# Optimization experiments

Hardware: AMD Instinct MI355X
Metric: run time of the kernel (lower is better)

## Reference

```python
import jax, jax.numpy as jnp
import numpy as np

HIDDEN = 1024
NUM_HEADS = 16
HEAD_DIM = HIDDEN // NUM_HEADS
LOCAL_WINDOW = 64
GLOBAL_WINDOW = 256
NEG_INF = -1.0e9


def _strided_mask(seq_len: int) -> jnp.ndarray:
    # Faithful vectorization of the torch loop:
    #   mask[i, max(0,i-w//2):min(S,i+w//2)] = 1  -> band j in [i-32, i+32)
    #   mask[i, ::stride] = 1, stride = max(1, S // global_window)
    i = jnp.arange(seq_len)[:, None]
    j = jnp.arange(seq_len)[None, :]
    half = LOCAL_WINDOW // 2
    local = (j >= i - half) & (j < i + half)
    stride = max(1, seq_len // GLOBAL_WINDOW)
    strided = (j % stride) == 0
    return local | strided  # bool [S, S]


def setup_inputs() -> dict:
    key = jax.random.key(0)
    ks = jax.random.split(key, 11)
    B, S, H = 2, 2048, HIDDEN
    scale = 1.0 / np.sqrt(H)
    inp = {
        "query": jax.random.normal(ks[0], (B, S, H), dtype=jnp.float32),
        "key": jax.random.normal(ks[1], (B, S, H), dtype=jnp.float32),
        "value": jax.random.normal(ks[2], (B, S, H), dtype=jnp.float32),
        # nn.Linear weights are [out, in]; y = x @ W.T + b
        "Wq": jax.random.normal(ks[3], (H, H), dtype=jnp.float32) * scale,
        "bq": jnp.zeros((H,), dtype=jnp.float32),
        "Wk": jax.random.normal(ks[4], (H, H), dtype=jnp.float32) * scale,
        "bk": jnp.zeros((H,), dtype=jnp.float32),
        "Wv": jax.random.normal(ks[5], (H, H), dtype=jnp.float32) * scale,
        "bv": jnp.zeros((H,), dtype=jnp.float32),
        "Wo": jax.random.normal(ks[6], (H, H), dtype=jnp.float32) * scale,
        "bo": jnp.zeros((H,), dtype=jnp.float32),
    }
    return inp


def reference(query, key, value, Wq, bq, Wk, bk, Wv, bv, Wo, bo):
    B, S, H = query.shape
    nH, dH = NUM_HEADS, HEAD_DIM
    scale = 1.0 / np.sqrt(dH)

    def split_heads(x):  # [B,S,H] -> [B,nH,S,dH]
        return x.reshape(B, S, nH, dH).transpose(0, 2, 1, 3)

    Q = split_heads(query @ Wq.T + bq)
    K = split_heads(key @ Wk.T + bk)
    V = split_heads(value @ Wv.T + bv)

    scores = jnp.einsum("bhqd,bhkd->bhqk", Q, K) * scale
    mask = _strided_mask(S)[None, None, :, :]
    scores = jnp.where(mask, scores, NEG_INF)
    attn = jax.nn.softmax(scores, axis=-1)
    # dropout is identity in eval mode
    context = jnp.einsum("bhqk,bhkd->bhqd", attn, V)
    context = context.transpose(0, 2, 1, 3).reshape(B, S, H)
    output = context @ Wo.T + bo
    return output, attn
```

## Files before the change

kernel.cpp:

```cpp
#include <hip/hip_runtime.h>

typedef unsigned int uint;
typedef unsigned short ushort_t;
typedef __bf16 bf16x8 __attribute__((ext_vector_type(8)));
typedef float f32x4 __attribute__((ext_vector_type(4)));

__device__ __forceinline__ int imin(int a, int b){ return a<b?a:b; }
__device__ __forceinline__ int imax(int a, int b){ return a>b?a:b; }

__device__ __forceinline__ ushort_t f2b(float f){
  uint u = __builtin_bit_cast(uint, f);
  u += 0x7FFFu + ((u>>16)&1u);
  return (ushort_t)(u>>16);
}
__device__ __forceinline__ float b2f(ushort_t s){
  uint u = ((uint)s)<<16;
  return __builtin_bit_cast(float, u);
}
__device__ __forceinline__ f32x4 fz4(){ f32x4 z; z[0]=0.f; z[1]=0.f; z[2]=0.f; z[3]=0.f; return z; }

__device__ __forceinline__ void gload16(const void* g, void* lds){
  __builtin_amdgcn_global_load_lds(
      (const __attribute__((address_space(1))) void*)g,
      (__attribute__((address_space(3))) void*)lds,
      16, 0, 0);
}

struct CJob { const float* src; ushort_t* dst; int nvec; };

__global__ __launch_bounds__(256) void convert_k(CJob j0, CJob j1, CJob j2,
                                                 CJob j3, CJob j4, CJob j5)
{
  CJob jb;
  switch (blockIdx.y){
    case 0: jb=j0; break; case 1: jb=j1; break; case 2: jb=j2; break;
    case 3: jb=j3; break; case 4: jb=j4; break; default: jb=j5; break;
  }
  int stride = gridDim.x*256;
  for (int i = blockIdx.x*256 + threadIdx.x; i < jb.nvec; i += stride){
    const float4* s = (const float4*)(jb.src + (size_t)i*8);
    float4 v0 = s[0], v1 = s[1];
    uint4 pk;
    pk.x = (uint)f2b(v0.x) | ((uint)f2b(v0.y)<<16);
    pk.y = (uint)f2b(v0.z) | ((uint)f2b(v0.w)<<16);
    pk.z = (uint)f2b(v1.x) | ((uint)f2b(v1.y)<<16);
    pk.w = (uint)f2b(v1.z) | ((uint)f2b(v1.w)<<16);
    *(uint4*)(jb.dst + (size_t)i*8) = pk;
  }
}

struct GArg { const ushort_t* A; const ushort_t* W; const float* bias; void* O; };

template<bool OBF16>
__global__ __launch_bounds__(256) void gemm_nt(GArg g0, GArg g1, GArg g2)
{
  GArg g = (blockIdx.z==0) ? g0 : ((blockIdx.z==1) ? g1 : g2);
  __shared__ __align__(16) ushort_t As[128*32];
  __shared__ __align__(16) ushort_t Bs[128*32];
  const int tid  = threadIdx.x;
  const int lane = tid & 63;
  const int w    = tid >> 6;
  const int ml   = lane & 15, quad = lane >> 4;

  int lid = blockIdx.x + 8*blockIdx.y;
  int t   = (lid & 7)*32 + (lid >> 3);
  const int m0 = (t >> 3)*128, n0 = (t & 7)*128;
  const int wm = (w>>1)*64, wn = (w&1)*64;

  const int srow = lane >> 2;
  const int scol = ((lane & 3) ^ ((lane >> 3) & 3))*8;
  const int rA0 = w*16, rA1 = 64 + w*16;
  const ushort_t* gA = g.A + (size_t)m0*1024;
  const ushort_t* gB = g.W + (size_t)n0*1024;
  const int sxor = (quad ^ ((ml >> 1) & 3))*8;

  f32x4 acc[4][4];
  #pragma unroll
  for (int i=0;i<4;i++)
    #pragma unroll
    for (int j=0;j<4;j++) acc[i][j]=fz4();

  for (int kt=0; kt<32; ++kt){
    int kof = kt*32 + scol;
    gload16(gA + (size_t)(rA0+srow)*1024 + kof, &As[rA0*32]);
    gload16(gA + (size_t)(rA1+srow)*1024 + kof, &As[rA1*32]);
    gload16(gB + (size_t)(rA0+srow)*1024 + kof, &Bs[rA0*32]);
    gload16(gB + (size_t)(rA1+srow)*1024 + kof, &Bs[rA1*32]);
    __syncthreads();

    bf16x8 af[4], bfr[4];
    #pragma unroll
    for (int t4=0;t4<4;t4++)
      af[t4]  = __builtin_bit_cast(bf16x8, *(const uint4*)&As[(wm + t4*16 + ml)*32 + sxor]);
    #pragma unroll
    for (int t4=0;t4<4;t4++)
      bfr[t4] = __builtin_bit_cast(bf16x8, *(const uint4*)&Bs[(wn + t4*16 + ml)*32 + sxor]);
    #pragma unroll
    for (int ti=0;ti<4;ti++)
      #pragma unroll
      for (int tj=0;tj<4;tj++)
        acc[ti][tj] = __builtin_amdgcn_mfma_f32_16x16x32_bf16(af[ti], bfr[tj], acc[ti][tj], 0,0,0);
    __syncthreads();
  }
  #pragma unroll
  for (int tj=0;tj<4;tj++){
    int gcol = n0 + wn + tj*16 + ml;
    float bv = g.bias[gcol];
    #pragma unroll
    for (int ti=0;ti<4;ti++){
      int growb = m0 + wm + ti*16 + quad*4;
      #pragma unroll
      for (int r=0;r<4;r++){
        float val = acc[ti][tj][r] + bv;
        size_t off = (size_t)(growb + r)*1024 + gcol;
        if (OBF16) ((ushort_t*)g.O)[off] = f2b(val);
        else       ((float*)g.O)[off]    = val;
      }
    }
  }
}

#define SW2 360
__global__ __launch_bounds__(128) void attn_k(
    const ushort_t* Qb, const ushort_t* Kb, const ushort_t* Vb,
    ushort_t* Ctxb, float* attn_out)
{
  __shared__ ushort_t stash[32*SW2];
  __shared__ float invl[32];
  const int lane = threadIdx.x & 63;
  const int w    = threadIdx.x >> 6;
  const int ml   = lane & 15, quad = lane >> 4;
  int lid = blockIdx.x + 64*(blockIdx.y + 16*blockIdx.z);
  int tt  = (lid & 7)*256 + (lid >> 3);
  const int tile = tt & 63, h = (tt >> 6) & 15, b = tt >> 10;
  const int i0  = tile*32;
  const int jl0 = i0 - 32;
  const int rb  = 16*w;
  const size_t bh = (size_t)b*2048*1024 + (size_t)h*64;

  bf16x8 aq0, aq1;
  {
    const ushort_t* qp = Qb + bh + (size_t)(i0 + rb + ml)*1024 + quad*8;
    aq0 = __builtin_bit_cast(bf16x8, *(const uint4*)qp);
    aq1 = __builtin_bit_cast(bf16x8, *(const uint4*)(qp + 32));
  }
  float lsum[4] = {0.f,0.f,0.f,0.f};
  for (int c=0;c<22;c++){
    int j  = (c<16) ? (128*c + 8*ml) : (jl0 + 16*(c-16) + ml);
    int jc = imin(imax(j,0),2047);
    const ushort_t* kp = Kb + bh + (size_t)jc*1024 + quad*8;
    bf16x8 kb0 = __builtin_bit_cast(bf16x8, *(const uint4*)kp);
    bf16x8 kb1 = __builtin_bit_cast(bf16x8, *(const uint4*)(kp + 32));
    f32x4 sc = fz4();
    sc = __builtin_amdgcn_mfma_f32_16x16x32_bf16(aq0, kb0, sc, 0,0,0);
    sc = __builtin_amdgcn_mfma_f32_16x16x32_bf16(aq1, kb1, sc, 0,0,0);
    int slot = 16*c + ml;
    #pragma unroll
    for (int r=0;r<4;r++){
      int rl = rb + quad*4 + r;
      int i  = i0 + rl;
      bool valid = (c<16) ? true :
        ((j>=0) && (j<2048) && ((j&7)!=0) && (j >= i-32) && (j < i+32));
      float e = valid ? __expf(sc[r]*0.125f) : 0.f;
      ushort_t eb = f2b(e);
      lsum[r] += b2f(eb);
      stash[rl*SW2 + slot] = eb;
    }
  }
  #pragma unroll
  for (int off=1; off<16; off<<=1){
    #pragma unroll
    for (int r=0;r<4;r++) lsum[r] += __shfl_xor(lsum[r], off);
  }
  if (ml==0){
    #pragma unroll
    for (int r=0;r<4;r++) invl[rb + quad*4 + r] = 1.f / lsum[r];
  }

  const size_t arow = ((size_t)(b*16 + h))*2048;
  for (int it=0; it<128; ++it){
    int r     = rb + (it>>3);
    int inner = ((it&7)<<6) + lane;
    int j0    = inner*4;
    float inv  = invl[r];
    float sval = b2f(stash[r*SW2 + (inner>>1)]);
    int off    = j0 - jl0;
    int offc   = imin(imax(off,0),92);
    uint2 lvu  = *(const uint2*)&stash[r*SW2 + 256 + offc];
    bool lok = (off>=0) && (off<96);
    float lx = lok ? b2f((ushort_t)(lvu.x & 0xffffu)) : 0.f;
    float ly = lok ? b2f((ushort_t)(lvu.x >> 16))     : 0.f;
    float lz = lok ? b2f((ushort_t)(lvu.y & 0xffffu)) : 0.f;
    float lw = lok ? b2f((ushort_t)(lvu.y >> 16))     : 0.f;
    f32x4 o;
    o[0] = ((inner&1)==0) ? inv*sval : inv*lx;
    o[1] = inv*ly; o[2] = inv*lz; o[3] = inv*lw;
    __builtin_nontemporal_store(o, (f32x4*)&attn_out[(arow + i0 + r)*2048 + j0]);
  }

  f32x4 pacc[4];
  #pragma unroll
  for (int nt=0;nt<4;nt++) pacc[nt]=fz4();
  const ushort_t* prow = &stash[(rb + ml)*SW2];
  for (int ck=0; ck<11; ++ck){
    int s0 = ck*32;
    bf16x8 pa = __builtin_bit_cast(bf16x8, *(const uint4*)(prow + s0 + quad*8));
    ushort_t vr[4][8];
    #pragma unroll
    for (int e=0;e<8;e++){
      int s = s0 + quad*8 + e;
      int j = (s<256) ? 8*s : (jl0 + s - 256);
      int jc = imin(imax(j,0),2047);
      const ushort_t* vp = Vb + bh + (size_t)jc*1024 + ml;
      #pragma unroll
      for (int nt=0;nt<4;nt++) vr[nt][e] = vp[nt*16];
    }
    #pragma unroll
    for (int nt=0;nt<4;nt++){
      uint4 pk;
      pk.x = (uint)vr[nt][0] | ((uint)vr[nt][1]<<16);
      pk.y = (uint)vr[nt][2] | ((uint)vr[nt][3]<<16);
      pk.z = (uint)vr[nt][4] | ((uint)vr[nt][5]<<16);
      pk.w = (uint)vr[nt][6] | ((uint)vr[nt][7]<<16);
      bf16x8 bfr = __builtin_bit_cast(bf16x8, pk);
      pacc[nt] = __builtin_amdgcn_mfma_f32_16x16x32_bf16(pa, bfr, pacc[nt], 0,0,0);
    }
  }
  #pragma unroll
  for (int nt=0;nt<4;nt++){
    #pragma unroll
    for (int rr=0;rr<4;rr++){
      int r = rb + quad*4 + rr;
      float val = pacc[nt][rr] * invl[r];
      Ctxb[bh + (size_t)(i0 + r)*1024 + nt*16 + ml] = f2b(val);
    }
  }
}

extern "C" void kernel_launch(void* const* d_in, const int* in_sizes, int n_in,
                              void* d_out, int out_size, void* d_ws, size_t ws_size,
                              hipStream_t stream) {
  (void)in_sizes; (void)n_in; (void)out_size; (void)ws_size;
  const float* query = (const float*)d_in[0];
  const float* key_  = (const float*)d_in[1];
  const float* value = (const float*)d_in[2];
  const float* Wq = (const float*)d_in[3];
  const float* bq = (const float*)d_in[4];
  const float* Wk = (const float*)d_in[5];
  const float* bk = (const float*)d_in[6];
  const float* Wv = (const float*)d_in[7];
  const float* bv = (const float*)d_in[8];
  const float* Wo = (const float*)d_in[9];
  const float* bo = (const float*)d_in[10];

  char* ws = (char*)d_ws;
  ushort_t* Qb   = (ushort_t*)(ws);
  ushort_t* Kb   = (ushort_t*)(ws + (size_t)( 8<<20));
  ushort_t* Vb   = (ushort_t*)(ws + (size_t)(16<<20));
  ushort_t* Ctxb = (ushort_t*)(ws + (size_t)(24<<20));

  float* out = (float*)d_out;
  float* attn_out = out + (size_t)4096*1024;

  ushort_t* scr = (ushort_t*)attn_out;
  ushort_t* Aq  = scr;
  ushort_t* Ak  = scr + (size_t)1*4096*1024;
  ushort_t* Av  = scr + (size_t)2*4096*1024;
  ushort_t* Wqb = scr + (size_t)3*4096*1024;
  ushort_t* Wkb = Wqb + (size_t)1024*1024;
  ushort_t* Wvb = Wkb + (size_t)1024*1024;
  ushort_t* Wob = Qb;

  const int NA = 4096*1024/8;
  const int NW = 1024*1024/8;

  CJob ja{query, Aq, NA}, jb{key_, Ak, NA}, jc{value, Av, NA};
  CJob jd{Wq, Wqb, NW}, je{Wk, Wkb, NW}, jf{Wv, Wvb, NW};
  convert_k<<<dim3(1024,6), 256, 0, stream>>>(ja, jb, jc, jd, je, jf);

  GArg ga{Aq, Wqb, bq, Qb};
  GArg gb{Ak, Wkb, bk, Kb};
  GArg gc{Av, Wvb, bv, Vb};
  gemm_nt<true><<<dim3(8,32,3), 256, 0, stream>>>(ga, gb, gc);

  attn_k<<<dim3(64,16,2), 128, 0, stream>>>(Qb, Kb, Vb, Ctxb, attn_out);

  CJob jo{Wo, Wob, NW};
  convert_k<<<dim3(512,1), 256, 0, stream>>>(jo, jo, jo, jo, jo, jo);

  GArg go{Ctxb, Wob, bo, out};
  gemm_nt<false><<<dim3(8,32,1), 256, 0, stream>>>(go, go, go);
}
```

Measured before the change: 703.5 us.

## Fuse Wo fp32-to-bf16 conversion into output GEMM and skip masked attn segments

Replaces the separate Wo conversion launch and output GEMM with a dedicated gemm_out kernel. It reads fp32 Wo directly, converts it to bf16 into LDS, and uses 128x64 tiles for more blocks. The attention-probability write loop now skips the local-window stash loads and conversions for 256-column segments that cannot overlap the local band, writing zeros directly. This removes one kernel launch and an intermediate round-trip, but the Wo tile is loaded synchronously in fp32 rather than with async LDS loads.

```diff
diff --git a/kernel.cpp b/kernel.cpp
--- a/kernel.cpp
+++ b/kernel.cpp
@@ -51,7 +51,6 @@
 
 struct GArg { const ushort_t* A; const ushort_t* W; const float* bias; void* O; };
 
-template<bool OBF16>
 __global__ __launch_bounds__(256) void gemm_nt(GArg g0, GArg g1, GArg g2)
 {
   GArg g = (blockIdx.z==0) ? g0 : ((blockIdx.z==1) ? g1 : g2);
@@ -112,10 +111,82 @@
       #pragma unroll
       for (int r=0;r<4;r++){
         float val = acc[ti][tj][r] + bv;
-        size_t off = (size_t)(growb + r)*1024 + gcol;
-        if (OBF16) ((ushort_t*)g.O)[off] = f2b(val);
-        else       ((float*)g.O)[off]    = val;
+        ((ushort_t*)g.O)[(size_t)(growb + r)*1024 + gcol] = f2b(val);
       }
+    }
+  }
+}
+
+__global__ __launch_bounds__(256) void gemm_out(
+    const ushort_t* A, const float* W, const float* bias, float* O)
+{
+  __shared__ __align__(16) ushort_t As[128*32];
+  __shared__ __align__(16) ushort_t Bs[64*32];
+  const int tid  = threadIdx.x;
+  const int lane = tid & 63;
+  const int w    = tid >> 6;
+  const int ml   = lane & 15, quad = lane >> 4;
+
+  int lid = blockIdx.x + 16*blockIdx.y;
+  int t   = (lid & 7)*64 + (lid >> 3);
+  const int m0 = (t >> 4)*128, n0 = (t & 15)*64;
+  const int wm = (w>>1)*64, wn = (w&1)*32;
+
+  const int srow = lane >> 2;
+  const int scol = ((lane & 3) ^ ((lane >> 3) & 3))*8;
+  const int rA0 = w*16, rA1 = 64 + w*16;
+  const ushort_t* gA = A + (size_t)m0*1024;
+  const int sxor = (quad ^ ((ml >> 1) & 3))*8;
+
+  const int brow = tid >> 2, bc = tid & 3;
+  const int bscol = (bc ^ ((brow >> 1) & 3))*8;
+  const float* gW = W + (size_t)(n0 + brow)*1024 + bc*8;
+
+  f32x4 acc[4][2];
+  #pragma unroll
+  for (int i=0;i<4;i++){ acc[i][0]=fz4(); acc[i][1]=fz4(); }
+
+  for (int kt=0; kt<32; ++kt){
+    int kof = kt*32 + scol;
+    gload16(gA + (size_t)(rA0+srow)*1024 + kof, &As[rA0*32]);
+    gload16(gA + (size_t)(rA1+srow)*1024 + kof, &As[rA1*32]);
+    {
+      const float* gw = gW + kt*32;
+      float4 v0 = *(const float4*)gw;
+      float4 v1 = *(const float4*)(gw+4);
+      uint4 pk;
+      pk.x = (uint)f2b(v0.x) | ((uint)f2b(v0.y)<<16);
+      pk.y = (uint)f2b(v0.z) | ((uint)f2b(v0.w)<<16);
+      pk.z = (uint)f2b(v1.x) | ((uint)f2b(v1.y)<<16);
+      pk.w = (uint)f2b(v1.z) | ((uint)f2b(v1.w)<<16);
+      *(uint4*)&Bs[brow*32 + bscol] = pk;
+    }
+    __syncthreads();
+
+    bf16x8 af[4], bfr[2];
+    #pragma unroll
+    for (int t4=0;t4<4;t4++)
+      af[t4]  = __builtin_bit_cast(bf16x8, *(const uint4*)&As[(wm + t4*16 + ml)*32 + sxor]);
+    #pragma unroll
+    for (int t4=0;t4<2;t4++)
+      bfr[t4] = __builtin_bit_cast(bf16x8, *(const uint4*)&Bs[(wn + t4*16 + ml)*32 + sxor]);
+    #pragma unroll
+    for (int ti=0;ti<4;ti++)
+      #pragma unroll
+      for (int tj=0;tj<2;tj++)
+        acc[ti][tj] = __builtin_amdgcn_mfma_f32_16x16x32_bf16(af[ti], bfr[tj], acc[ti][tj], 0,0,0);
+    __syncthreads();
+  }
+  #pragma unroll
+  for (int tj=0;tj<2;tj++){
+    int gcol = n0 + wn + tj*16 + ml;
+    float bv = bias[gcol];
+    #pragma unroll
+    for (int ti=0;ti<4;ti++){
+      int growb = m0 + wm + ti*16 + quad*4;
+      #pragma unroll
+      for (int r=0;r<4;r++)
+        O[(size_t)(growb + r)*1024 + gcol] = acc[ti][tj][r] + bv;
     }
   }
 }
@@ -180,21 +251,28 @@
   const size_t arow = ((size_t)(b*16 + h))*2048;
   for (int it=0; it<128; ++it){
     int r     = rb + (it>>3);
-    int inner = ((it&7)<<6) + lane;
+    int seg   = it & 7;
+    int inner = (seg<<6) + lane;
     int j0    = inner*4;
     float inv  = invl[r];
     float sval = b2f(stash[r*SW2 + (inner>>1)]);
-    int off    = j0 - jl0;
-    int offc   = imin(imax(off,0),92);
-    uint2 lvu  = *(const uint2*)&stash[r*SW2 + 256 + offc];
-    bool lok = (off>=0) && (off<96);
-    float lx = lok ? b2f((ushort_t)(lvu.x & 0xffffu)) : 0.f;
-    float ly = lok ? b2f((ushort_t)(lvu.x >> 16))     : 0.f;
-    float lz = lok ? b2f((ushort_t)(lvu.y & 0xffffu)) : 0.f;
-    float lw = lok ? b2f((ushort_t)(lvu.y >> 16))     : 0.f;
     f32x4 o;
-    o[0] = ((inner&1)==0) ? inv*sval : inv*lx;
-    o[1] = inv*ly; o[2] = inv*lz; o[3] = inv*lw;
+    bool segLocal = (seg*256 < jl0 + 96) && (seg*256 + 256 > jl0);
+    if (segLocal){
+      int off  = j0 - jl0;
+      int offc = imin(imax(off,0),92);
+      uint2 lvu = *(const uint2*)&stash[r*SW2 + 256 + offc];
+      bool lok = (off>=0) && (off<96);
+      float lx = lok ? b2f((ushort_t)(lvu.x & 0xffffu)) : 0.f;
+      float ly = lok ? b2f((ushort_t)(lvu.x >> 16))     : 0.f;
+      float lz = lok ? b2f((ushort_t)(lvu.y & 0xffffu)) : 0.f;
+      float lw = lok ? b2f((ushort_t)(lvu.y >> 16))     : 0.f;
+      o[0] = ((inner&1)==0) ? inv*sval : inv*lx;
+      o[1] = inv*ly; o[2] = inv*lz; o[3] = inv*lw;
+    } else {
+      o[0] = ((inner&1)==0) ? inv*sval : 0.f;
+      o[1] = 0.f; o[2] = 0.f; o[3] = 0.f;
+    }
     __builtin_nontemporal_store(o, (f32x4*)&attn_out[(arow + i0 + r)*2048 + j0]);
   }
 
@@ -269,7 +347,6 @@
   ushort_t* Wqb = scr + (size_t)3*4096*1024;
   ushort_t* Wkb = Wqb + (size_t)1024*1024;
   ushort_t* Wvb = Wkb + (size_t)1024*1024;
-  ushort_t* Wob = Qb;
 
   const int NA = 4096*1024/8;
   const int NW = 1024*1024/8;
@@ -281,13 +358,9 @@
   GArg ga{Aq, Wqb, bq, Qb};
   GArg gb{Ak, Wkb, bk, Kb};
   GArg gc{Av, Wvb, bv, Vb};
-  gemm_nt<true><<<dim3(8,32,3), 256, 0, stream>>>(ga, gb, gc);
+  gemm_nt<<<dim3(8,32,3), 256, 0, stream>>>(ga, gb, gc);
 
   attn_k<<<dim3(64,16,2), 128, 0, stream>>>(Qb, Kb, Vb, Ctxb, attn_out);
 
-  CJob jo{Wo, Wob, NW};
-  convert_k<<<dim3(512,1), 256, 0, stream>>>(jo, jo, jo, jo, jo, jo);
-
-  GArg go{Ctxb, Wob, bo, out};
-  gemm_nt<false><<<dim3(8,32,1), 256, 0, stream>>>(go, go, go);
-}
+  gemm_out<<<dim3(16,32), 256, 0, stream>>>(Ctxb, Wo, bo, out);
+}
```

After: 721.0 us. +2.5%, slower.
